# Kernel tuning notes

Hardware: AMD Instinct MI355X
Metric: run time of the kernel (lower is better)

## Reference

```python
import jax, jax.numpy as jnp
import numpy as np

N_NODES = 50000
N_EDGES = 800000
HIDDEN = 64


def _init_linear(key, fan_in, fan_out):
    kw, kb = jax.random.split(key)
    lim = 1.0 / np.sqrt(fan_in)
    W = jax.random.uniform(kw, (fan_in, fan_out), jnp.float32, -lim, lim)
    b = jax.random.uniform(kb, (fan_out,), jnp.float32, -lim, lim)
    return W, b


def setup_inputs() -> dict:
    key = jax.random.key(0)
    ks = jax.random.split(key, 10)
    feat = jax.random.normal(ks[0], (N_NODES, HIDDEN), jnp.float32)
    x = jax.random.normal(ks[1], (N_NODES, 3), jnp.float32)
    src = jax.random.randint(ks[2], (N_EDGES,), 0, N_NODES, jnp.int32)
    dst = jax.random.randint(ks[3], (N_EDGES,), 0, N_NODES, jnp.int32)
    # message MLP: (2H+1) -> H -> H, relu after both layers (last_activation=mid)
    W1, b1 = _init_linear(ks[4], 2 * HIDDEN + 1, HIDDEN)
    W2, b2 = _init_linear(ks[5], HIDDEN, HIDDEN)
    # soft edge gate: H -> 1
    we, be = _init_linear(ks[6], HIDDEN, 1)
    # update MLP: H -> H -> H, relu mid, no last activation
    U1, c1 = _init_linear(ks[7], HIDDEN, HIDDEN)
    U2, c2 = _init_linear(ks[8], HIDDEN, HIDDEN)
    return dict(feat=feat, x=x, src=src, dst=dst,
                W1=W1, b1=b1, W2=W2, b2=b2, we=we, be=be,
                U1=U1, c1=c1, U2=U2, c2=c2)


def reference(feat, x, src, dst, W1, b1, W2, b2, we, be, U1, c1, U2, c2):
    # per-edge squared distance between endpoint coordinates: [E, 1]
    sqd = jnp.sum((x[src] - x[dst]) ** 2, axis=-1, keepdims=True)
    # message input: [E, 2H+1]
    msg_in = jnp.concatenate([feat[src], feat[dst], sqd], axis=-1)
    # 2-layer message MLP with relu mid and last activation
    m = jax.nn.relu(jax.nn.relu(msg_in @ W1 + b1) @ W2 + b2)
    # sigmoid soft-edge gate: [E, 1]
    gate = jax.nn.sigmoid(m @ we + be)
    # scatter-sum gated messages to destination nodes: [N, H]
    m_sum = jax.ops.segment_sum(m * gate, dst, num_segments=N_NODES)
    # node update MLP on (m_sum + feat), residual add
    h = m_sum + feat
    h_new = jax.nn.relu(h @ U1 + c1) @ U2 + c2
    return h_new + feat
```

## Files before the change

### kernel.cpp

```cpp
#include <hip/hip_runtime.h>
#include <hip/hip_bf16.h>
#include <stdint.h>

#define N_NODES 50000
#define N_EDGES 800000
#define HDIM 64
#define SCAN_N (N_NODES + 1)

#define MSUM_OFF   0
#define EP_OFF     12800000
#define DEG_OFF    (EP_OFF + 12800000)
#define OFFS_OFF   (DEG_OFF + 204800)
#define POS_OFF    (OFFS_OFF + 204800)
#define FB_OFF     (POS_OFF + 204800)
#define W1T_OFF    (FB_OFF + (size_t)N_NODES * HDIM * 2)
#define W2T_OFF    (W1T_OFF + 16384)
#define U1T_OFF    (W2T_OFF + 8192)
#define U2T_OFF    (U1T_OFF + 8192)
#define WS_NEED    (U2T_OFF + 8192)

#define CVT_BLOCKS   1563
#define PREPW_BLOCKS 80
#define MZ_BLOCKS    3125
#define HIST_BLOCKS  1024

typedef __attribute__((ext_vector_type(8))) short short8;
typedef __attribute__((ext_vector_type(4))) float floatx4;

__device__ __forceinline__ float bf2f(unsigned short u) {
    union { unsigned int i; float f; } v; v.i = ((unsigned int)u) << 16; return v.f;
}
__device__ __forceinline__ unsigned short f2bf(float f) {
    __hip_bfloat16 h = __float2bfloat16(f);
    return *reinterpret_cast<unsigned short*>(&h);
}

__device__ __forceinline__ int detect_is_bf16(const unsigned short* p) {
    int cnt = 0;
    #pragma unroll
    for (int i = 0; i < 64; ++i) {
        unsigned short b = p[i];
        int e = (b >> 7) & 0xFF;
        cnt += ((e >= 97 && e <= 157) || (b & 0x7FFF) == 0) ? 1 : 0;
    }
    return cnt >= 56;
}

__device__ __forceinline__ float getf(const void* p, unsigned int i, int isb) {
    return isb ? bf2f(((const unsigned short*)p)[i]) : ((const float*)p)[i];
}

__device__ __forceinline__ short8 get8bf(const void* p, unsigned int i, int isb) {
    if (isb) {
        return *reinterpret_cast<const short8*>((const short*)p + i);
    } else {
        const float4 f0 = *reinterpret_cast<const float4*>((const float*)p + i);
        const float4 f1 = *reinterpret_cast<const float4*>((const float*)p + i + 4);
        short8 a;
        a[0] = (short)f2bf(f0.x); a[1] = (short)f2bf(f0.y);
        a[2] = (short)f2bf(f0.z); a[3] = (short)f2bf(f0.w);
        a[4] = (short)f2bf(f1.x); a[5] = (short)f2bf(f1.y);
        a[6] = (short)f2bf(f1.z); a[7] = (short)f2bf(f1.w);
        return a;
    }
}

#define COMPILER_FENCE() asm volatile("" ::: "memory")
#define WAIT_LDS() __builtin_amdgcn_s_waitcnt(0xC07F)

__global__ __launch_bounds__(256) void prep_kernel(
    const void* __restrict__ feat, unsigned short* __restrict__ fb,
    const void* __restrict__ W1, const void* __restrict__ W2,
    const void* __restrict__ U1, const void* __restrict__ U2,
    unsigned short* __restrict__ w1t, unsigned short* __restrict__ w2t,
    unsigned short* __restrict__ u1t, unsigned short* __restrict__ u2t,
    const int* __restrict__ dst, int* __restrict__ deg,
    uint4* __restrict__ msumz)
{
    const int b = blockIdx.x;
    if (b < CVT_BLOCKS) {
        const int isb = detect_is_bf16((const unsigned short*)feat);
        int i = (b * 256 + threadIdx.x) * 8;
        if (i >= N_NODES * HDIM) return;
        if (isb) {
            *reinterpret_cast<uint4*>(fb + i) =
                *reinterpret_cast<const uint4*>((const unsigned short*)feat + i);
        } else {
            float4 f0 = *reinterpret_cast<const float4*>((const float*)feat + i);
            float4 f1 = *reinterpret_cast<const float4*>((const float*)feat + i + 4);
            ushort4 a = {f2bf(f0.x), f2bf(f0.y), f2bf(f0.z), f2bf(f0.w)};
            ushort4 c = {f2bf(f1.x), f2bf(f1.y), f2bf(f1.z), f2bf(f1.w)};
            *reinterpret_cast<ushort4*>(fb + i)     = a;
            *reinterpret_cast<ushort4*>(fb + i + 4) = c;
        }
    } else if (b < CVT_BLOCKS + PREPW_BLOCKS) {
        const int isb = detect_is_bf16((const unsigned short*)feat);
        int idx = (b - CVT_BLOCKS) * 256 + threadIdx.x;
        if (idx < 8192) {
            int n = idx >> 7, k = idx & 127;
            w1t[idx] = f2bf(getf(W1, k * 64 + n, isb));
        } else if (idx < 12288) {
            int i = idx - 8192, n = i >> 6, k = i & 63;
            w2t[i] = f2bf(getf(W2, k * 64 + n, isb));
        } else if (idx < 16384) {
            int i = idx - 12288, n = i >> 6, k = i & 63;
            u1t[i] = f2bf(getf(U1, k * 64 + n, isb));
        } else if (idx < 20480) {
            int i = idx - 16384, n = i >> 6, k = i & 63;
            u2t[i] = f2bf(getf(U2, k * 64 + n, isb));
        }
    } else if (b < CVT_BLOCKS + PREPW_BLOCKS + MZ_BLOCKS) {
        int i = (b - CVT_BLOCKS - PREPW_BLOCKS) * 256 + threadIdx.x;
        if (i < N_NODES * HDIM / 4)
            msumz[i] = (uint4){0u, 0u, 0u, 0u};
    } else {
        int e0 = (b - CVT_BLOCKS - PREPW_BLOCKS - MZ_BLOCKS) * 256 + threadIdx.x;
        for (int e = e0; e < N_EDGES; e += HIST_BLOCKS * 256)
            atomicAdd(&deg[dst[e]], 1);
    }
}

__global__ void scan1_kernel(const int* __restrict__ deg, int* __restrict__ part) {
    __shared__ int s[1024];
    int g = blockIdx.x * 1024 + threadIdx.x;
    s[threadIdx.x] = (g < SCAN_N) ? deg[g] : 0;
    __syncthreads();
    for (int off = 512; off > 0; off >>= 1) {
        if (threadIdx.x < off) s[threadIdx.x] += s[threadIdx.x + off];
        __syncthreads();
    }
    if (threadIdx.x == 0) part[blockIdx.x] = s[0];
}

__global__ void scan2_kernel(int* __restrict__ part, int nparts) {
    if (threadIdx.x == 0) {
        int run = 0;
        for (int i = 0; i < nparts; ++i) { int t = part[i]; part[i] = run; run += t; }
    }
}

__global__ void scan3_kernel(const int* __restrict__ deg, const int* __restrict__ part,
                             int* __restrict__ offs, int* __restrict__ pos) {
    __shared__ int s[1024];
    int g = blockIdx.x * 1024 + threadIdx.x;
    int v = (g < SCAN_N) ? deg[g] : 0;
    s[threadIdx.x] = v;
    __syncthreads();
    for (int off = 1; off < 1024; off <<= 1) {
        int t = (threadIdx.x >= off) ? s[threadIdx.x - off] : 0;
        __syncthreads();
        s[threadIdx.x] += t;
        __syncthreads();
    }
    int excl = s[threadIdx.x] - v + part[blockIdx.x];
    if (g < SCAN_N) { offs[g] = excl; pos[g] = excl; }
}

__global__ __launch_bounds__(256) void permute_kernel(
    const void* __restrict__ feat, const void* __restrict__ xpos,
    const int* __restrict__ src, const int* __restrict__ dst,
    int* __restrict__ pos, uint4* __restrict__ epack)
{
    const int isb = detect_is_bf16((const unsigned short*)feat);
    int e = blockIdx.x * 256 + threadIdx.x;
    if (e < N_EDGES) {
        int s = src[e], d = dst[e];
        int slot = atomicAdd(&pos[d], 1);
        float dx = getf(xpos, s * 3 + 0, isb) - getf(xpos, d * 3 + 0, isb);
        float dy = getf(xpos, s * 3 + 1, isb) - getf(xpos, d * 3 + 1, isb);
        float dz = getf(xpos, s * 3 + 2, isb) - getf(xpos, d * 3 + 2, isb);
        float sqd = dx * dx + dy * dy + dz * dz;
        uint4 p;
        p.x = (unsigned int)s;
        p.y = (unsigned int)d;
        p.z = __float_as_uint(sqd);
        p.w = 0u;
        epack[slot] = p;
    }
}

template <bool CSR>
__global__ __launch_bounds__(512, 6) void edge_kernel(
    const unsigned short* __restrict__ fbf,
    const unsigned short* __restrict__ w1t, const unsigned short* __restrict__ w2t,
    const void* __restrict__ feat, const void* __restrict__ xpos,
    const int* __restrict__ src, const int* __restrict__ dst,
    const uint4* __restrict__ epack,
    const void* __restrict__ W1, const void* __restrict__ b1,
    const void* __restrict__ W2, const void* __restrict__ b2,
    const void* __restrict__ we, const void* __restrict__ be,
    float* __restrict__ msum, unsigned int msum_cap)
{
    __shared__ __align__(16) short sW1[16][64][8];
    __shared__ __align__(16) short sW2[8][64][8];
    __shared__ __align__(16) short sA2[8][16][72];

    const int isb  = detect_is_bf16((const unsigned short*)feat);
    const int tid  = threadIdx.x;
    const int wave = tid >> 6;
    const int lane = tid & 63;
    const int l15  = lane & 15;
    const int quad = lane >> 4;

    short8 bw1[4][4];
    short8 bw2[2][4];
    if (CSR) {
        for (int i = tid; i < 16 * 64; i += 512) {
            int f = i >> 6, l = i & 63;
            int n = (f & 3) * 16 + (l & 15);
            int k0 = (f >> 2) * 32 + (l >> 4) * 8;
            *reinterpret_cast<short8*>(&sW1[f][l][0]) =
                *reinterpret_cast<const short8*>(w1t + n * 128 + k0);
        }
        for (int i = tid; i < 8 * 64; i += 512) {
            int f = i >> 6, l = i & 63;
            int n = (f & 3) * 16 + (l & 15);
            int k0 = (f >> 2) * 32 + (l >> 4) * 8;
            *reinterpret_cast<short8*>(&sW2[f][l][0]) =
                *reinterpret_cast<const short8*>(w2t + n * 64 + k0);
        }
        __syncthreads();
    } else {
        #pragma unroll
        for (int c = 0; c < 4; ++c)
            #pragma unroll
            for (int nt = 0; nt < 4; ++nt) {
                short8 b;
                #pragma unroll
                for (int j = 0; j < 8; ++j)
                    b[j] = (short)f2bf(getf(W1, (c * 32 + quad * 8 + j) * 64 + nt * 16 + l15, isb));
                bw1[c][nt] = b;
            }
        #pragma unroll
        for (int c = 0; c < 2; ++c)
            #pragma unroll
            for (int nt = 0; nt < 4; ++nt) {
                short8 b;
                #pragma unroll
                for (int j = 0; j < 8; ++j)
                    b[j] = (short)f2bf(getf(W2, (c * 32 + quad * 8 + j) * 64 + nt * 16 + l15, isb));
                bw2[c][nt] = b;
            }
    }

    float b1r[4], w1lr[4], b2r[4], wer[4];
    #pragma unroll
    for (int nt = 0; nt < 4; ++nt) {
        int n = nt * 16 + l15;
        b1r[nt]  = getf(b1, n, isb);
        w1lr[nt] = getf(W1, 128 * 64 + n, isb);
        b2r[nt]  = getf(b2, n, isb);
        wer[nt]  = getf(we, n, isb);
    }
    const float ber = getf(be, 0, isb);
    const int rowb = quad * 4;

    const int ntiles = N_EDGES / 128;
    for (int t = blockIdx.x; t < ntiles; t += gridDim.x) {
        const int ebase = t * 128 + wave * 16;

        int sidx = 0, didx = 0;
        float sqd = 0.f;
        if (CSR) {
            if (lane < 16) {
                uint4 p = epack[ebase + lane];
                sidx = (int)p.x;
                didx = (int)p.y;
                sqd  = __uint_as_float(p.z);
            }
        } else {
            if (lane < 16) {
                int e = ebase + lane;
                sidx = src[e];
                didx = dst[e];
                float dx = getf(xpos, sidx * 3 + 0, isb) - getf(xpos, didx * 3 + 0, isb);
                float dy = getf(xpos, sidx * 3 + 1, isb) - getf(xpos, didx * 3 + 1, isb);
                float dz = getf(xpos, sidx * 3 + 2, isb) - getf(xpos, didx * 3 + 2, isb);
                sqd = dx * dx + dy * dy + dz * dz;
            }
        }
        const int sn     = __shfl(sidx, l15);
        const int dn_row = __shfl(didx, l15);

        floatx4 acc[4];
        #pragma unroll
        for (int nt = 0; nt < 4; ++nt) acc[nt] = (floatx4){0.f, 0.f, 0.f, 0.f};
        #pragma unroll
        for (int c = 0; c < 4; ++c) {
            const int node = (c < 2) ? sn : dn_row;
            const unsigned int aoff = (unsigned int)node * 64u + (c & 1) * 32 + quad * 8;
            short8 a;
            if (CSR) a = *reinterpret_cast<const short8*>((const short*)fbf + aoff);
            else     a = get8bf(feat, aoff, isb);
            #pragma unroll
            for (int nt = 0; nt < 4; ++nt) {
                short8 b;
                if (CSR) b = *reinterpret_cast<const short8*>(&sW1[c * 4 + nt][lane][0]);
                else     b = bw1[c][nt];
                acc[nt] = __builtin_amdgcn_mfma_f32_16x16x32_bf16(a, b, acc[nt], 0, 0, 0);
            }
        }

        float sq[4];
        #pragma unroll
        for (int r = 0; r < 4; ++r) sq[r] = __shfl(sqd, rowb + r);
        #pragma unroll
        for (int nt = 0; nt < 4; ++nt)
            #pragma unroll
            for (int r = 0; r < 4; ++r) {
                float v = fmaxf(acc[nt][r] + b1r[nt] + sq[r] * w1lr[nt], 0.f);
                sA2[wave][rowb + r][nt * 16 + l15] = (short)f2bf(v);
            }
        COMPILER_FENCE();
        WAIT_LDS();

        floatx4 acc2[4];
        #pragma unroll
        for (int nt = 0; nt < 4; ++nt) acc2[nt] = (floatx4){0.f, 0.f, 0.f, 0.f};
        #pragma unroll
        for (int c = 0; c < 2; ++c) {
            short8 a = *reinterpret_cast<const short8*>(&sA2[wave][l15][c * 32 + quad * 8]);
            #pragma unroll
            for (int nt = 0; nt < 4; ++nt) {
                short8 b;
                if (CSR) b = *reinterpret_cast<const short8*>(&sW2[c * 4 + nt][lane][0]);
                else     b = bw2[c][nt];
                acc2[nt] = __builtin_amdgcn_mfma_f32_16x16x32_bf16(a, b, acc2[nt], 0, 0, 0);
            }
        }
        COMPILER_FENCE();

        float mval[4][4];
        float part[4] = {0.f, 0.f, 0.f, 0.f};
        #pragma unroll
        for (int nt = 0; nt < 4; ++nt)
            #pragma unroll
            for (int r = 0; r < 4; ++r) {
                float v = fmaxf(acc2[nt][r] + b2r[nt], 0.f);
                mval[nt][r] = v;
                part[r] += v * wer[nt];
            }
        #pragma unroll
        for (int off = 1; off < 16; off <<= 1)
            #pragma unroll
            for (int r = 0; r < 4; ++r) part[r] += __shfl_xor(part[r], off);
        float gate[4];
        #pragma unroll
        for (int r = 0; r < 4; ++r)
            gate[r] = 1.f / (1.f + __expf(-(part[r] + ber)));

        if (CSR) {
            int nd = __shfl(didx, (lane + 1) & 15);
            int flag = (lane == 15) || (nd != didx);
            unsigned long long bal = __ballot(lane < 16 && flag);
            unsigned int m16 = (unsigned int)(bal & 0xFFFFull);
            int lo = 0;
            while (m16) {
                int hi = __ffs(m16) - 1;
                float s0 = 0.f, s1 = 0.f, s2 = 0.f, s3 = 0.f;
                #pragma unroll
                for (int r = 0; r < 4; ++r) {
                    int gr = rowb + r;
                    float g = (gr >= lo && gr <= hi) ? gate[r] : 0.f;
                    s0 += g * mval[0][r];
                    s1 += g * mval[1][r];
                    s2 += g * mval[2][r];
                    s3 += g * mval[3][r];
                }
                s0 += __shfl_xor(s0, 16); s0 += __shfl_xor(s0, 32);
                s1 += __shfl_xor(s1, 16); s1 += __shfl_xor(s1, 32);
                s2 += __shfl_xor(s2, 16); s2 += __shfl_xor(s2, 32);
                s3 += __shfl_xor(s3, 16); s3 += __shfl_xor(s3, 32);
                int d = __shfl(didx, hi);
                float v = (quad == 0) ? s0 : (quad == 1) ? s1 : (quad == 2) ? s2 : s3;
                unsafeAtomicAdd(&msum[(unsigned int)d * 64u + (unsigned int)quad * 16u + l15], v);
                lo = hi + 1;
                m16 &= m16 - 1;
            }
        } else {
            #pragma unroll
            for (int r = 0; r < 4; ++r) {
                int dn = __shfl(didx, rowb + r);
                unsigned int base = (unsigned int)dn * 64u;
                if (base + 64u <= msum_cap) {
                    #pragma unroll
                    for (int nt = 0; nt < 4; ++nt)
                        unsafeAtomicAdd(&msum[base + nt * 16 + l15], mval[nt][r] * gate[r]);
                }
            }
        }
    }
}

__global__ __launch_bounds__(256, 2) void node_kernel(
    const float* __restrict__ msum,
    const unsigned short* __restrict__ u1t, const unsigned short* __restrict__ u2t,
    const void* __restrict__ feat,
    const void* __restrict__ U1, const void* __restrict__ c1v,
    const void* __restrict__ U2, const void* __restrict__ c2v,
    void* __restrict__ out)
{
    __shared__ __align__(16) short sT[4][16][72];
    __shared__ __align__(16) float sF[4][16][68];

    const int isb  = detect_is_bf16((const unsigned short*)feat);
    const int tid  = threadIdx.x;
    const int wave = tid >> 6;
    const int lane = tid & 63;
    const int l15  = lane & 15;
    const int quad = lane >> 4;

    short8 u1f[2][4], u2f[2][4];
    if (u1t) {
        #pragma unroll
        for (int nt = 0; nt < 4; ++nt) {
            const int n = nt * 16 + l15;
            #pragma unroll
            for (int c = 0; c < 2; ++c) {
                u1f[c][nt] = *reinterpret_cast<const short8*>(u1t + n * 64 + c * 32 + quad * 8);
                u2f[c][nt] = *reinterpret_cast<const short8*>(u2t + n * 64 + c * 32 + quad * 8);
            }
        }
    } else {
        #pragma unroll
        for (int c = 0; c < 2; ++c)
            #pragma unroll
            for (int nt = 0; nt < 4; ++nt) {
                short8 a, b;
                #pragma unroll
                for (int j = 0; j < 8; ++j) {
                    int k = c * 32 + quad * 8 + j, n = nt * 16 + l15;
                    a[j] = (short)f2bf(getf(U1, k * 64 + n, isb));
                    b[j] = (short)f2bf(getf(U2, k * 64 + n, isb));
                }
                u1f[c][nt] = a; u2f[c][nt] = b;
            }
    }
    float c1r[4], c2r[4];
    #pragma unroll
    for (int nt = 0; nt < 4; ++nt) {
        c1r[nt] = getf(c1v, nt * 16 + l15, isb);
        c2r[nt] = getf(c2v, nt * 16 + l15, isb);
    }
    const int rowb = quad * 4;

    const int ntile = (N_NODES + 15) / 16;
    const int t = blockIdx.x * 4 + wave;
    if (t < ntile) {
        const int node = t * 16 + l15;

        short8 ah[2];
        #pragma unroll
        for (int c = 0; c < 2; ++c) {
            unsigned int off = (unsigned int)node * 64u + c * 32 + quad * 8;
            float4 m0 = *reinterpret_cast<const float4*>(msum + off);
            float4 m1 = *reinterpret_cast<const float4*>(msum + off + 4);
            float mv[8] = {m0.x, m0.y, m0.z, m0.w, m1.x, m1.y, m1.z, m1.w};
            float hv[8];
            if (isb) {
                short8 fv = *reinterpret_cast<const short8*>((const short*)feat + off);
                #pragma unroll
                for (int j = 0; j < 8; ++j) hv[j] = bf2f((unsigned short)fv[j]);
            } else {
                float4 f0 = *reinterpret_cast<const float4*>((const float*)feat + off);
                float4 f1 = *reinterpret_cast<const float4*>((const float*)feat + off + 4);
                hv[0] = f0.x; hv[1] = f0.y; hv[2] = f0.z; hv[3] = f0.w;
                hv[4] = f1.x; hv[5] = f1.y; hv[6] = f1.z; hv[7] = f1.w;
            }
            short8 a;
            #pragma unroll
            for (int j = 0; j < 8; ++j) a[j] = (short)f2bf(mv[j] + hv[j]);
            ah[c] = a;
        }

        floatx4 acc[4];
        #pragma unroll
        for (int nt = 0; nt < 4; ++nt) acc[nt] = (floatx4){0.f, 0.f, 0.f, 0.f};
        #pragma unroll
        for (int c = 0; c < 2; ++c)
            #pragma unroll
            for (int nt = 0; nt < 4; ++nt)
                acc[nt] = __builtin_amdgcn_mfma_f32_16x16x32_bf16(ah[c], u1f[c][nt], acc[nt], 0, 0, 0);

        #pragma unroll
        for (int nt = 0; nt < 4; ++nt)
            #pragma unroll
            for (int r = 0; r < 4; ++r) {
                float v = fmaxf(acc[nt][r] + c1r[nt], 0.f);
                sT[wave][rowb + r][nt * 16 + l15] = (short)f2bf(v);
            }
        COMPILER_FENCE();
        WAIT_LDS();

        floatx4 acc2[4];
        #pragma unroll
        for (int nt = 0; nt < 4; ++nt) acc2[nt] = (floatx4){0.f, 0.f, 0.f, 0.f};
        #pragma unroll
        for (int c = 0; c < 2; ++c) {
            short8 a = *reinterpret_cast<const short8*>(&sT[wave][l15][c * 32 + quad * 8]);
            #pragma unroll
            for (int nt = 0; nt < 4; ++nt)
                acc2[nt] = __builtin_amdgcn_mfma_f32_16x16x32_bf16(a, u2f[c][nt], acc2[nt], 0, 0, 0);
        }
        COMPILER_FENCE();

        #pragma unroll
        for (int nt = 0; nt < 4; ++nt)
            #pragma unroll
            for (int r = 0; r < 4; ++r)
                sF[wave][rowb + r][nt * 16 + l15] = acc2[nt][r] + c2r[nt];
        COMPILER_FENCE();
        WAIT_LDS();

        const unsigned int ob = (unsigned int)node * 64u + quad * 16;
        if (isb) {
            const unsigned short* fp = (const unsigned short*)feat + ob;
            unsigned short* op = (unsigned short*)out + ob;
            #pragma unroll
            for (int k = 0; k < 2; ++k) {
                ushort4 o0, o1;
                float4 v0 = *reinterpret_cast<const float4*>(&sF[wave][l15][quad * 16 + k * 8]);
                float4 v1 = *reinterpret_cast<const float4*>(&sF[wave][l15][quad * 16 + k * 8 + 4]);
                const ushort4 f0 = *reinterpret_cast<const ushort4*>(fp + k * 8);
                const ushort4 f1 = *reinterpret_cast<const ushort4*>(fp + k * 8 + 4);
                o0.x = f2bf(v0.x + bf2f(f0.x)); o0.y = f2bf(v0.y + bf2f(f0.y));
                o0.z = f2bf(v0.z + bf2f(f0.z)); o0.w = f2bf(v0.w + bf2f(f0.w));
                o1.x = f2bf(v1.x + bf2f(f1.x)); o1.y = f2bf(v1.y + bf2f(f1.y));
                o1.z = f2bf(v1.z + bf2f(f1.z)); o1.w = f2bf(v1.w + bf2f(f1.w));
                *reinterpret_cast<ushort4*>(op + k * 8)     = o0;
                *reinterpret_cast<ushort4*>(op + k * 8 + 4) = o1;
            }
        } else {
            const float* fp = (const float*)feat + ob;
            float* op = (float*)out + ob;
            #pragma unroll
            for (int k = 0; k < 4; ++k) {
                float4 v = *reinterpret_cast<const float4*>(&sF[wave][l15][quad * 16 + k * 4]);
                float4 f = *reinterpret_cast<const float4*>(fp + k * 4);
                float4 o = {v.x + f.x, v.y + f.y, v.z + f.z, v.w + f.w};
                *reinterpret_cast<float4*>(op + k * 4) = o;
            }
        }
        COMPILER_FENCE();
    }
}

extern "C" void kernel_launch(void* const* d_in, const int* in_sizes, int n_in,
                              void* d_out, int out_size, void* d_ws, size_t ws_size,
                              hipStream_t stream) {
    const void* feat = d_in[0];
    const void* x    = d_in[1];
    const int* src   = (const int*)d_in[2];
    const int* dst   = (const int*)d_in[3];
    const void* W1   = d_in[4];
    const void* b1   = d_in[5];
    const void* W2   = d_in[6];
    const void* b2   = d_in[7];
    const void* we   = d_in[8];
    const void* be   = d_in[9];
    const void* U1   = d_in[10];
    const void* c1   = d_in[11];
    const void* U2   = d_in[12];
    const void* c2   = d_in[13];
    char* ws = (char*)d_ws;

    if (ws_size >= WS_NEED) {
        float* msum = (float*)(ws + MSUM_OFF);
        uint4* epack = (uint4*)(ws + EP_OFF);
        int* deg  = (int*)(ws + DEG_OFF);
        int* offs = (int*)(ws + OFFS_OFF);
        int* pos  = (int*)(ws + POS_OFF);
        unsigned short* fb  = (unsigned short*)(ws + FB_OFF);
        unsigned short* w1t = (unsigned short*)(ws + W1T_OFF);
        unsigned short* w2t = (unsigned short*)(ws + W2T_OFF);
        unsigned short* u1t = (unsigned short*)(ws + U1T_OFF);
        unsigned short* u2t = (unsigned short*)(ws + U2T_OFF);

        hipMemsetAsync(deg, 0, 204800, stream);
        prep_kernel<<<CVT_BLOCKS + PREPW_BLOCKS + MZ_BLOCKS + HIST_BLOCKS, 256, 0, stream>>>(
            feat, fb, W1, W2, U1, U2, w1t, w2t, u1t, u2t, dst, deg, (uint4*)msum);
        scan1_kernel<<<49, 1024, 0, stream>>>(deg, offs + 51200 - 64);
        scan2_kernel<<<1, 64, 0, stream>>>(offs + 51200 - 64, 49);
        scan3_kernel<<<49, 1024, 0, stream>>>(deg, offs + 51200 - 64, offs, pos);
        permute_kernel<<<(N_EDGES + 255) / 256, 256, 0, stream>>>(feat, x, src, dst, pos, epack);
        edge_kernel<true><<<1250, 512, 0, stream>>>(fb, w1t, w2t, feat, x, src, dst, epack,
                                                    W1, b1, W2, b2, we, be,
                                                    msum, (unsigned int)(N_NODES * HDIM));
        node_kernel<<<((N_NODES + 15) / 16 + 3) / 4, 256, 0, stream>>>(
            msum, u1t, u2t, feat, U1, c1, U2, c2, d_out);
    } else {
        float* msum = (float*)ws;
        size_t need = (size_t)N_NODES * HDIM * sizeof(float);
        size_t clr  = need < ws_size ? need : ws_size;
        unsigned int cap = (unsigned int)(ws_size / sizeof(float));
        if (cap > (unsigned int)(N_NODES * HDIM)) cap = (unsigned int)(N_NODES * HDIM);

        hipMemsetAsync(msum, 0, clr, stream);
        edge_kernel<false><<<1250, 512, 0, stream>>>(nullptr, nullptr, nullptr, feat, x, src, dst,
                                                     nullptr, W1, b1, W2, b2, we, be,
                                                     msum, cap);
        node_kernel<<<((N_NODES + 15) / 16 + 3) / 4, 256, 0, stream>>>(
            msum, nullptr, nullptr, feat, U1, c1, U2, c2, d_out);
    }
}
```

Before: 263.0 us.

## Process two 16-edge tiles per wave, merge scan into one pass, precompute constants

The edge kernel now has each wave handle two interleaved 16-edge groups per iteration, with two independent MFMA chains and doubled LDS staging. The aim is more instruction-level parallelism and better hiding of gather latency; the grid is halved and launch bounds are relaxed to allow more registers. Bias and gate constants are precomputed once into a small float buffer in the prep kernel, so edge blocks no longer run the per-block dtype detection and scalar loads. The three scan kernels are replaced by one single-block wave-shuffle scan, removing two launches but serialising the scan across 49 segments in one block.

After: 296.0 us. 1.13x slower.

```diff
diff --git a/kernel.cpp b/kernel.cpp
--- a/kernel.cpp
+++ b/kernel.cpp
@@ -17,10 +17,11 @@
 #define W2T_OFF    (W1T_OFF + 16384)
 #define U1T_OFF    (W2T_OFF + 8192)
 #define U2T_OFF    (U1T_OFF + 8192)
-#define WS_NEED    (U2T_OFF + 8192)
+#define CST_OFF    (U2T_OFF + 8192)
+#define WS_NEED    (CST_OFF + 4096)
 
 #define CVT_BLOCKS   1563
-#define PREPW_BLOCKS 80
+#define PREPW_BLOCKS 82
 #define MZ_BLOCKS    3125
 #define HIST_BLOCKS  1024
 
@@ -72,8 +73,11 @@
     const void* __restrict__ feat, unsigned short* __restrict__ fb,
     const void* __restrict__ W1, const void* __restrict__ W2,
     const void* __restrict__ U1, const void* __restrict__ U2,
+    const void* __restrict__ b1, const void* __restrict__ b2,
+    const void* __restrict__ we, const void* __restrict__ be,
     unsigned short* __restrict__ w1t, unsigned short* __restrict__ w2t,
     unsigned short* __restrict__ u1t, unsigned short* __restrict__ u2t,
+    float* __restrict__ cst,
     const int* __restrict__ dst, int* __restrict__ deg,
     uint4* __restrict__ msumz)
 {
@@ -108,6 +112,15 @@
         } else if (idx < 20480) {
             int i = idx - 16384, n = i >> 6, k = i & 63;
             u2t[i] = f2bf(getf(U2, k * 64 + n, isb));
+        } else if (idx < 20737) {
+            int i = idx - 20480;
+            float v;
+            if (i < 64)       v = getf(b1, i, isb);
+            else if (i < 128) v = getf(W1, 128 * 64 + (i - 64), isb);
+            else if (i < 192) v = getf(b2, i - 128, isb);
+            else if (i < 256) v = getf(we, i - 192, isb);
+            else              v = getf(be, 0, isb);
+            cst[i] = v;
         }
     } else if (b < CVT_BLOCKS + PREPW_BLOCKS + MZ_BLOCKS) {
         int i = (b - CVT_BLOCKS - PREPW_BLOCKS) * 256 + threadIdx.x;
@@ -120,40 +133,42 @@
     }
 }
 
-__global__ void scan1_kernel(const int* __restrict__ deg, int* __restrict__ part) {
-    __shared__ int s[1024];
-    int g = blockIdx.x * 1024 + threadIdx.x;
-    s[threadIdx.x] = (g < SCAN_N) ? deg[g] : 0;
-    __syncthreads();
-    for (int off = 512; off > 0; off >>= 1) {
-        if (threadIdx.x < off) s[threadIdx.x] += s[threadIdx.x + off];
+__global__ __launch_bounds__(1024) void scan_onepass_kernel(
+    const int* __restrict__ deg, int* __restrict__ offs, int* __restrict__ pos)
+{
+    __shared__ int wsum[16];
+    const int tid  = threadIdx.x;
+    const int wid  = tid >> 6;
+    const int lane = tid & 63;
+    int run = 0;
+    for (int seg = 0; seg < 49; ++seg) {
+        int g = seg * 1024 + tid;
+        int v = (g < SCAN_N) ? deg[g] : 0;
+        int x = v;
+        #pragma unroll
+        for (int off = 1; off < 64; off <<= 1) {
+            int t = __shfl_up(x, off);
+            if (lane >= off) x += t;
+        }
+        if (lane == 63) wsum[wid] = x;
         __syncthreads();
-    }
-    if (threadIdx.x == 0) part[blockIdx.x] = s[0];
-}
-
-__global__ void scan2_kernel(int* __restrict__ part, int nparts) {
-    if (threadIdx.x == 0) {
-        int run = 0;
-        for (int i = 0; i < nparts; ++i) { int t = part[i]; part[i] = run; run += t; }
-    }
-}
-
-__global__ void scan3_kernel(const int* __restrict__ deg, const int* __restrict__ part,
-                             int* __restrict__ offs, int* __restrict__ pos) {
-    __shared__ int s[1024];
-    int g = blockIdx.x * 1024 + threadIdx.x;
-    int v = (g < SCAN_N) ? deg[g] : 0;
-    s[threadIdx.x] = v;
-    __syncthreads();
-    for (int off = 1; off < 1024; off <<= 1) {
-        int t = (threadIdx.x >= off) ? s[threadIdx.x - off] : 0;
+        if (wid == 0) {
+            int w = (lane < 16) ? wsum[lane] : 0;
+            #pragma unroll
+            for (int off = 1; off < 16; off <<= 1) {
+                int t = __shfl_up(w, off);
+                if (lane >= off) w += t;
+            }
+            if (lane < 16) wsum[lane] = w;
+        }
         __syncthreads();
-        s[threadIdx.x] += t;
+        int wexcl = (wid == 0) ? 0 : wsum[wid - 1];
+        int tot   = wsum[15];
+        int excl  = run + wexcl + (x - v);
+        if (g < SCAN_N) { offs[g] = excl; pos[g] = excl; }
+        run += tot;
         __syncthreads();
     }
-    int excl = s[threadIdx.x] - v + part[blockIdx.x];
-    if (g < SCAN_N) { offs[g] = excl; pos[g] = excl; }
 }
 
 __global__ __launch_bounds__(256) void permute_kernel(
@@ -180,9 +195,10 @@
 }
 
 template <bool CSR>
-__global__ __launch_bounds__(512, 6) void edge_kernel(
+__global__ __launch_bounds__(512, 4) void edge_kernel(
     const unsigned short* __restrict__ fbf,
     const unsigned short* __restrict__ w1t, const unsigned short* __restrict__ w2t,
+    const float* __restrict__ cst,
     const void* __restrict__ feat, const void* __restrict__ xpos,
     const int* __restrict__ src, const int* __restrict__ dst,
     const uint4* __restrict__ epack,
@@ -193,18 +209,21 @@
 {
     __shared__ __align__(16) short sW1[16][64][8];
     __shared__ __align__(16) short sW2[8][64][8];
-    __shared__ __align__(16) short sA2[8][16][72];
-
-    const int isb  = detect_is_bf16((const unsigned short*)feat);
+    __shared__ __align__(16) short sA2[2][8][16][72];
+
     const int tid  = threadIdx.x;
     const int wave = tid >> 6;
     const int lane = tid & 63;
     const int l15  = lane & 15;
     const int quad = lane >> 4;
-
+    const int rowb = quad * 4;
+
+    float b1r[4], w1lr[4], b2r[4], wer[4];
+    float ber;
     short8 bw1[4][4];
     short8 bw2[2][4];
-    if (CSR) {
+
+    if constexpr (CSR) {
         for (int i = tid; i < 16 * 64; i += 512) {
             int f = i >> 6, l = i & 63;
             int n = (f & 3) * 16 + (l & 15);
@@ -219,8 +238,183 @@
             *reinterpret_cast<short8*>(&sW2[f][l][0]) =
                 *reinterpret_cast<const short8*>(w2t + n * 64 + k0);
         }
+        #pragma unroll
+        for (int nt = 0; nt < 4; ++nt) {
+            int n = nt * 16 + l15;
+            b1r[nt]  = cst[n];
+            w1lr[nt] = cst[64 + n];
+            b2r[nt]  = cst[128 + n];
+            wer[nt]  = cst[192 + n];
+        }
+        ber = cst[256];
         __syncthreads();
+
+        const int nbiter = N_EDGES / 256;
+        for (int it = blockIdx.x; it < nbiter; it += gridDim.x) {
+            const int ebase = it * 256 + wave * 16;
+
+            int sidx = 0, didx = 0;
+            float sqd = 0.f;
+            if (lane < 32) {
+                int e = ebase + l15 + ((lane >> 4) << 7);
+                uint4 p = epack[e];
+                sidx = (int)p.x;
+                didx = (int)p.y;
+                sqd  = __uint_as_float(p.z);
+            }
+            const int snA = __shfl(sidx, l15);
+            const int dnA = __shfl(didx, l15);
+            const int snB = __shfl(sidx, l15 + 16);
+            const int dnB = __shfl(didx, l15 + 16);
+
+            short8 caA[4], caB[4];
+            #pragma unroll
+            for (int c = 0; c < 4; ++c) {
+                const int nA = (c < 2) ? snA : dnA;
+                const int nB = (c < 2) ? snB : dnB;
+                caA[c] = *reinterpret_cast<const short8*>(
+                    (const short*)fbf + (unsigned int)nA * 64u + (c & 1) * 32 + quad * 8);
+                caB[c] = *reinterpret_cast<const short8*>(
+                    (const short*)fbf + (unsigned int)nB * 64u + (c & 1) * 32 + quad * 8);
+            }
+
+            floatx4 accA[4], accB[4];
+            #pragma unroll
+            for (int nt = 0; nt < 4; ++nt) {
+                accA[nt] = (floatx4){0.f, 0.f, 0.f, 0.f};
+                accB[nt] = (floatx4){0.f, 0.f, 0.f, 0.f};
+            }
+            #pragma unroll
+            for (int c = 0; c < 4; ++c) {
+                #pragma unroll
+                for (int nt = 0; nt < 4; ++nt) {
+                    short8 wb = *reinterpret_cast<const short8*>(&sW1[c * 4 + nt][lane][0]);
+                    accA[nt] = __builtin_amdgcn_mfma_f32_16x16x32_bf16(caA[c], wb, accA[nt], 0, 0, 0);
+                    accB[nt] = __builtin_amdgcn_mfma_f32_16x16x32_bf16(caB[c], wb, accB[nt], 0, 0, 0);
+                }
+            }
+
+            float sqA[4], sqB[4];
+            #pragma unroll
+            for (int r = 0; r < 4; ++r) {
+                sqA[r] = __shfl(sqd, rowb + r);
+                sqB[r] = __shfl(sqd, 16 + rowb + r);
+            }
+            #pragma unroll
+            for (int nt = 0; nt < 4; ++nt)
+                #pragma unroll
+                for (int r = 0; r < 4; ++r) {
+                    float vA = fmaxf(accA[nt][r] + b1r[nt] + sqA[r] * w1lr[nt], 0.f);
+                    float vB = fmaxf(accB[nt][r] + b1r[nt] + sqB[r] * w1lr[nt], 0.f);
+                    sA2[0][wave][rowb + r][nt * 16 + l15] = (short)f2bf(vA);
+                    sA2[1][wave][rowb + r][nt * 16 + l15] = (short)f2bf(vB);
+                }
+            COMPILER_FENCE();
+            WAIT_LDS();
+
+            floatx4 acc2A[4], acc2B[4];
+            #pragma unroll
+            for (int nt = 0; nt < 4; ++nt) {
+                acc2A[nt] = (floatx4){0.f, 0.f, 0.f, 0.f};
+                acc2B[nt] = (floatx4){0.f, 0.f, 0.f, 0.f};
+            }
+            #pragma unroll
+            for (int c = 0; c < 2; ++c) {
+                short8 aA = *reinterpret_cast<const short8*>(&sA2[0][wave][l15][c * 32 + quad * 8]);
+                short8 aB = *reinterpret_cast<const short8*>(&sA2[1][wave][l15][c * 32 + quad * 8]);
+                #pragma unroll
+                for (int nt = 0; nt < 4; ++nt) {
+                    short8 wb = *reinterpret_cast<const short8*>(&sW2[c * 4 + nt][lane][0]);
+                    acc2A[nt] = __builtin_amdgcn_mfma_f32_16x16x32_bf16(aA, wb, acc2A[nt], 0, 0, 0);
+                    acc2B[nt] = __builtin_amdgcn_mfma_f32_16x16x32_bf16(aB, wb, acc2B[nt], 0, 0, 0);
+                }
+            }
+            COMPILER_FENCE();
+
+            float mvA[4][4], mvB[4][4];
+            float pA[4] = {0.f, 0.f, 0.f, 0.f};
+            float pB[4] = {0.f, 0.f, 0.f, 0.f};
+            #pragma unroll
+            for (int nt = 0; nt < 4; ++nt)
+                #pragma unroll
+                for (int r = 0; r < 4; ++r) {
+                    float vA = fmaxf(acc2A[nt][r] + b2r[nt], 0.f);
+                    float vB = fmaxf(acc2B[nt][r] + b2r[nt], 0.f);
+                    mvA[nt][r] = vA;
+                    mvB[nt][r] = vB;
+                    pA[r] += vA * wer[nt];
+                    pB[r] += vB * wer[nt];
+                }
+            #pragma unroll
+            for (int off = 1; off < 16; off <<= 1)
+                #pragma unroll
+                for (int r = 0; r < 4; ++r) {
+                    pA[r] += __shfl_xor(pA[r], off);
+                    pB[r] += __shfl_xor(pB[r], off);
+                }
+            float gA[4], gB[4];
+            #pragma unroll
+            for (int r = 0; r < 4; ++r) {
+                gA[r] = 1.f / (1.f + __expf(-(pA[r] + ber)));
+                gB[r] = 1.f / (1.f + __expf(-(pB[r] + ber)));
+            }
+
+            int grp = (lane >> 4) & 1;
+            int nd = __shfl(didx, grp * 16 + ((l15 + 1) & 15));
+            int flag = (lane < 32) && ((l15 == 15) || (nd != didx));
+            unsigned long long bal = __ballot(flag);
+            unsigned int mA = (unsigned int)(bal & 0xFFFFull);
+            unsigned int mB = (unsigned int)((bal >> 16) & 0xFFFFull);
+
+            int lo = 0;
+            while (mA) {
+                int hi = __ffs(mA) - 1;
+                float s0 = 0.f, s1 = 0.f, s2 = 0.f, s3 = 0.f;
+                #pragma unroll
+                for (int r = 0; r < 4; ++r) {
+                    int gr = rowb + r;
+                    float g = (gr >= lo && gr <= hi) ? gA[r] : 0.f;
+                    s0 += g * mvA[0][r];
+                    s1 += g * mvA[1][r];
+                    s2 += g * mvA[2][r];
+                    s3 += g * mvA[3][r];
+                }
+                s0 += __shfl_xor(s0, 16); s0 += __shfl_xor(s0, 32);
+                s1 += __shfl_xor(s1, 16); s1 += __shfl_xor(s1, 32);
+                s2 += __shfl_xor(s2, 16); s2 += __shfl_xor(s2, 32);
+                s3 += __shfl_xor(s3, 16); s3 += __shfl_xor(s3, 32);
+                int d = __shfl(didx, hi);
+                float v = (quad == 0) ? s0 : (quad == 1) ? s1 : (quad == 2) ? s2 : s3;
+                unsafeAtomicAdd(&msum[(unsigned int)d * 64u + (unsigned int)quad * 16u + l15], v);
+                lo = hi + 1;
+                mA &= mA - 1;
+            }
+            lo = 0;
+            while (mB) {
+                int hi = __ffs(mB) - 1;
+                float s0 = 0.f, s1 = 0.f, s2 = 0.f, s3 = 0.f;
+                #pragma unroll
+                for (int r = 0; r < 4; ++r) {
+                    int gr = rowb + r;
+                    float g = (gr >= lo && gr <= hi) ? gB[r] : 0.f;
+                    s0 += g * mvB[0][r];
+                    s1 += g * mvB[1][r];
+                    s2 += g * mvB[2][r];
+                    s3 += g * mvB[3][r];
+                }
+                s0 += __shfl_xor(s0, 16); s0 += __shfl_xor(s0, 32);
+                s1 += __shfl_xor(s1, 16); s1 += __shfl_xor(s1, 32);
+                s2 += __shfl_xor(s2, 16); s2 += __shfl_xor(s2, 32);
+                s3 += __shfl_xor(s3, 16); s3 += __shfl_xor(s3, 32);
+                int d = __shfl(didx, 16 + hi);
+                float v = (quad == 0) ? s0 : (quad == 1) ? s1 : (quad == 2) ? s2 : s3;
+                unsafeAtomicAdd(&msum[(unsigned int)d * 64u + (unsigned int)quad * 16u + l15], v);
+                lo = hi + 1;
+                mB &= mB - 1;
+            }
+        }
     } else {
+        const int isb = detect_is_bf16((const unsigned short*)feat);
         #pragma unroll
         for (int c = 0; c < 4; ++c)
             #pragma unroll
@@ -241,34 +435,21 @@
                     b[j] = (short)f2bf(getf(W2, (c * 32 + quad * 8 + j) * 64 + nt * 16 + l15, isb));
                 bw2[c][nt] = b;
             }
-    }
-
-    float b1r[4], w1lr[4], b2r[4], wer[4];
-    #pragma unroll
-    for (int nt = 0; nt < 4; ++nt) {
-        int n = nt * 16 + l15;
-        b1r[nt]  = getf(b1, n, isb);
-        w1lr[nt] = getf(W1, 128 * 64 + n, isb);
-        b2r[nt]  = getf(b2, n, isb);
-        wer[nt]  = getf(we, n, isb);
-    }
-    const float ber = getf(be, 0, isb);
-    const int rowb = quad * 4;
-
-    const int ntiles = N_EDGES / 128;
-    for (int t = blockIdx.x; t < ntiles; t += gridDim.x) {
-        const int ebase = t * 128 + wave * 16;
-
-        int sidx = 0, didx = 0;
-        float sqd = 0.f;
-        if (CSR) {
-            if (lane < 16) {
-                uint4 p = epack[ebase + lane];
-                sidx = (int)p.x;
-                didx = (int)p.y;
-                sqd  = __uint_as_float(p.z);
-            }
-        } else {
+        #pragma unroll
+        for (int nt = 0; nt < 4; ++nt) {
+            int n = nt * 16 + l15;
+            b1r[nt]  = getf(b1, n, isb);
+            w1lr[nt] = getf(W1, 128 * 64 + n, isb);
+            b2r[nt]  = getf(b2, n, isb);
+            wer[nt]  = getf(we, n, isb);
+        }
+        ber = getf(be, 0, isb);
+
+        const int ntiles = N_EDGES / 128;
+        for (int t = blockIdx.x; t < ntiles; t += gridDim.x) {
+            const int ebase = t * 128 + wave * 16;
+            int sidx = 0, didx = 0;
+            float sqd = 0.f;
             if (lane < 16) {
                 int e = ebase + lane;
                 sidx = src[e];
@@ -278,106 +459,66 @@
                 float dz = getf(xpos, sidx * 3 + 2, isb) - getf(xpos, didx * 3 + 2, isb);
                 sqd = dx * dx + dy * dy + dz * dz;
             }
-        }
-        const int sn     = __shfl(sidx, l15);
-        const int dn_row = __shfl(didx, l15);
-
-        floatx4 acc[4];
-        #pragma unroll
-        for (int nt = 0; nt < 4; ++nt) acc[nt] = (floatx4){0.f, 0.f, 0.f, 0.f};
-        #pragma unroll
-        for (int c = 0; c < 4; ++c) {
-            const int node = (c < 2) ? sn : dn_row;
-            const unsigned int aoff = (unsigned int)node * 64u + (c & 1) * 32 + quad * 8;
-            short8 a;
-            if (CSR) a = *reinterpret_cast<const short8*>((const short*)fbf + aoff);
-            else     a = get8bf(feat, aoff, isb);
-            #pragma unroll
-            for (int nt = 0; nt < 4; ++nt) {
-                short8 b;
-                if (CSR) b = *reinterpret_cast<const short8*>(&sW1[c * 4 + nt][lane][0]);
-                else     b = bw1[c][nt];
-                acc[nt] = __builtin_amdgcn_mfma_f32_16x16x32_bf16(a, b, acc[nt], 0, 0, 0);
-            }
-        }
-
-        float sq[4];
-        #pragma unroll
-        for (int r = 0; r < 4; ++r) sq[r] = __shfl(sqd, rowb + r);
-        #pragma unroll
-        for (int nt = 0; nt < 4; ++nt)
-            #pragma unroll
-            for (int r = 0; r < 4; ++r) {
-                float v = fmaxf(acc[nt][r] + b1r[nt] + sq[r] * w1lr[nt], 0.f);
-                sA2[wave][rowb + r][nt * 16 + l15] = (short)f2bf(v);
-            }
-        COMPILER_FENCE();
-        WAIT_LDS();
-
-        floatx4 acc2[4];
-        #pragma unroll
-        for (int nt = 0; nt < 4; ++nt) acc2[nt] = (floatx4){0.f, 0.f, 0.f, 0.f};
-        #pragma unroll
-        for (int c = 0; c < 2; ++c) {
-            short8 a = *reinterpret_cast<const short8*>(&sA2[wave][l15][c * 32 + quad * 8]);
-            #pragma unroll
-            for (int nt = 0; nt < 4; ++nt) {
-                short8 b;
-                if (CSR) b = *reinterpret_cast<const short8*>(&sW2[c * 4 + nt][lane][0]);
-                else     b = bw2[c][nt];
-                acc2[nt] = __builtin_amdgcn_mfma_f32_16x16x32_bf16(a, b, acc2[nt], 0, 0, 0);
-            }
-        }
-        COMPILER_FENCE();
-
-        float mval[4][4];
-        float part[4] = {0.f, 0.f, 0.f, 0.f};
-        #pragma unroll
-        for (int nt = 0; nt < 4; ++nt)
-            #pragma unroll
-            for (int r = 0; r < 4; ++r) {
-                float v = fmaxf(acc2[nt][r] + b2r[nt], 0.f);
-                mval[nt][r] = v;
-                part[r] += v * wer[nt];
-            }
-        #pragma unroll
-        for (int off = 1; off < 16; off <<= 1)
-            #pragma unroll
-            for (int r = 0; r < 4; ++r) part[r] += __shfl_xor(part[r], off);
-        float gate[4];
-        #pragma unroll
-        for (int r = 0; r < 4; ++r)
-            gate[r] = 1.f / (1.f + __expf(-(part[r] + ber)));
-
-        if (CSR) {
-            int nd = __shfl(didx, (lane + 1) & 15);
-            int flag = (lane == 15) || (nd != didx);
-            unsigned long long bal = __ballot(lane < 16 && flag);
-            unsigned int m16 = (unsigned int)(bal & 0xFFFFull);
-            int lo = 0;
-            while (m16) {
-                int hi = __ffs(m16) - 1;
-                float s0 = 0.f, s1 = 0.f, s2 = 0.f, s3 = 0.f;
+            const int sn     = __shfl(sidx, l15);
+            const int dn_row = __shfl(didx, l15);
+
+            floatx4 acc[4];
+            #pragma unroll
+            for (int nt = 0; nt < 4; ++nt) acc[nt] = (floatx4){0.f, 0.f, 0.f, 0.f};
+            #pragma unroll
+            for (int c = 0; c < 4; ++c) {
+                const int node = (c < 2) ? sn : dn_row;
+                const unsigned int aoff = (unsigned int)node * 64u + (c & 1) * 32 + quad * 8;
+                short8 a = get8bf(feat, aoff, isb);
+                #pragma unroll
+                for (int nt = 0; nt < 4; ++nt)
+                    acc[nt] = __builtin_amdgcn_mfma_f32_16x16x32_bf16(a, bw1[c][nt], acc[nt], 0, 0, 0);
+            }
+
+            float sq[4];
+            #pragma unroll
+            for (int r = 0; r < 4; ++r) sq[r] = __shfl(sqd, rowb + r);
+            #pragma unroll
+            for (int nt = 0; nt < 4; ++nt)
                 #pragma unroll
                 for (int r = 0; r < 4; ++r) {
-                    int gr = rowb + r;
-                    float g = (gr >= lo && gr <= hi) ? gate[r] : 0.f;
-                    s0 += g * mval[0][r];
-                    s1 += g * mval[1][r];
-                    s2 += g * mval[2][r];
-                    s3 += g * mval[3][r];
-                }
-                s0 += __shfl_xor(s0, 16); s0 += __shfl_xor(s0, 32);
-                s1 += __shfl_xor(s1, 16); s1 += __shfl_xor(s1, 32);
-                s2 += __shfl_xor(s2, 16); s2 += __shfl_xor(s2, 32);
-                s3 += __shfl_xor(s3, 16); s3 += __shfl_xor(s3, 32);
-                int d = __shfl(didx, hi);
-                float v = (quad == 0) ? s0 : (quad == 1) ? s1 : (quad == 2) ? s2 : s3;
-                unsafeAtomicAdd(&msum[(unsigned int)d * 64u + (unsigned int)quad * 16u + l15], v);
-                lo = hi + 1;
-                m16 &= m16 - 1;
-            }
-        } else {
+                    float v = fmaxf(acc[nt][r] + b1r[nt] + sq[r] * w1lr[nt], 0.f);
+                    sA2[0][wave][rowb + r][nt * 16 + l15] = (short)f2bf(v);
+                }
+            COMPILER_FENCE();
+            WAIT_LDS();
+
+            floatx4 acc2[4];
+            #pragma unroll
+            for (int nt = 0; nt < 4; ++nt) acc2[nt] = (floatx4){0.f, 0.f, 0.f, 0.f};
+            #pragma unroll
+            for (int c = 0; c < 2; ++c) {
+                short8 a = *reinterpret_cast<const short8*>(&sA2[0][wave][l15][c * 32 + quad * 8]);
+                #pragma unroll
+                for (int nt = 0; nt < 4; ++nt)
+                    acc2[nt] = __builtin_amdgcn_mfma_f32_16x16x32_bf16(a, bw2[c][nt], acc2[nt], 0, 0, 0);
+            }
+            COMPILER_FENCE();
+
+            float mval[4][4];
+            float part[4] = {0.f, 0.f, 0.f, 0.f};
+            #pragma unroll
+            for (int nt = 0; nt < 4; ++nt)
+                #pragma unroll
+                for (int r = 0; r < 4; ++r) {
+                    float v = fmaxf(acc2[nt][r] + b2r[nt], 0.f);
+                    mval[nt][r] = v;
+                    part[r] += v * wer[nt];
+                }
+            #pragma unroll
+            for (int off = 1; off < 16; off <<= 1)
+                #pragma unroll
+                for (int r = 0; r < 4; ++r) part[r] += __shfl_xor(part[r], off);
+            float gate[4];
+            #pragma unroll
+            for (int r = 0; r < 4; ++r)
+                gate[r] = 1.f / (1.f + __expf(-(part[r] + ber)));
+
             #pragma unroll
             for (int r = 0; r < 4; ++r) {
                 int dn = __shfl(didx, rowb + r);
@@ -575,17 +716,17 @@
         unsigned short* w2t = (unsigned short*)(ws + W2T_OFF);
         unsigned short* u1t = (unsigned short*)(ws + U1T_OFF);
         unsigned short* u2t = (unsigned short*)(ws + U2T_OFF);
+        float* cst = (float*)(ws + CST_OFF);
 
         hipMemsetAsync(deg, 0, 204800, stream);
         prep_kernel<<<CVT_BLOCKS + PREPW_BLOCKS + MZ_BLOCKS + HIST_BLOCKS, 256, 0, stream>>>(
-            feat, fb, W1, W2, U1, U2, w1t, w2t, u1t, u2t, dst, deg, (uint4*)msum);
-        scan1_kernel<<<49, 1024, 0, stream>>>(deg, offs + 51200 - 64);
-        scan2_kernel<<<1, 64, 0, stream>>>(offs + 51200 - 64, 49);
-        scan3_kernel<<<49, 1024, 0, stream>>>(deg, offs + 51200 - 64, offs, pos);
+            feat, fb, W1, W2, U1, U2, b1, b2, we, be,
+            w1t, w2t, u1t, u2t, cst, dst, deg, (uint4*)msum);
+        scan_onepass_kernel<<<1, 1024, 0, stream>>>(deg, offs, pos);
         permute_kernel<<<(N_EDGES + 255) / 256, 256, 0, stream>>>(feat, x, src, dst, pos, epack);
-        edge_kernel<true><<<1250, 512, 0, stream>>>(fb, w1t, w2t, feat, x, src, dst, epack,
-                                                    W1, b1, W2, b2, we, be,
-                                                    msum, (unsigned int)(N_NODES * HDIM));
+        edge_kernel<true><<<625, 512, 0, stream>>>(fb, w1t, w2t, cst, feat, x, src, dst, epack,
+                                                   W1, b1, W2, b2, we, be,
+                                                   msum, (unsigned int)(N_NODES * HDIM));
         node_kernel<<<((N_NODES + 15) / 16 + 3) / 4, 256, 0, stream>>>(
             msum, u1t, u2t, feat, U1, c1, U2, c2, d_out);
     } else {
@@ -596,7 +737,8 @@
         if (cap > (unsigned int)(N_NODES * HDIM)) cap = (unsigned int)(N_NODES * HDIM);
 
         hipMemsetAsync(msum, 0, clr, stream);
-        edge_kernel<false><<<1250, 512, 0, stream>>>(nullptr, nullptr, nullptr, feat, x, src, dst,
+        edge_kernel<false><<<1250, 512, 0, stream>>>(nullptr, nullptr, nullptr, nullptr,
+                                                     feat, x, src, dst,
                                                      nullptr, W1, b1, W2, b2, we, be,
                                                      msum, cap);
         node_kernel<<<((N_NODES + 15) / 16 + 3) / 4, 256, 0, stream>>>(
```
